# Kernel optimization log

Measured on AMD Instinct MI355X. Metric: run time of the kernel, lower is better.

## Reference

```python
import jax, jax.numpy as jnp
import numpy as np
import math

DIM = 1024
N_HEADS = 16
HEAD_DIM = DIM // N_HEADS
MAX_LEN = 4096
THETA = 10000.0
LN_EPS = 1e-5


def _rope_tables(dim, max_len, theta=THETA):
    # matches precompute_rope: freqs over even indices, angles = outer(t, freqs)
    inv = 1.0 / theta ** (np.arange(0, dim, 2, dtype=np.float32) / dim)
    t = np.arange(max_len, dtype=np.float32)
    ang = np.outer(t, inv)  # [max_len, dim//2]
    return jnp.asarray(np.cos(ang)), jnp.asarray(np.sin(ang))


def setup_inputs() -> dict:
    key = jax.random.key(0)
    ks = jax.random.split(key, 5)
    B, T, D = 2, 2048, DIM
    s = 1.0 / math.sqrt(D)
    x = jax.random.normal(ks[0], (B, T, D), dtype=jnp.float32)
    wq = jax.random.normal(ks[1], (D, D), dtype=jnp.float32) * s
    wk = jax.random.normal(ks[2], (D, D), dtype=jnp.float32) * s
    wv = jax.random.normal(ks[3], (D, D), dtype=jnp.float32) * s
    wo = jax.random.normal(ks[4], (D, D), dtype=jnp.float32) * s
    ln_g = jnp.ones((D,), dtype=jnp.float32)
    ln_b = jnp.zeros((D,), dtype=jnp.float32)
    cos, sin = _rope_tables(HEAD_DIM, MAX_LEN)
    return {"x": x, "wq": wq, "wk": wk, "wv": wv, "wo": wo,
            "ln_g": ln_g, "ln_b": ln_b, "cos": cos, "sin": sin}


def _rotate(x, cos, sin):
    # x: [B, T, H, hd]; complex multiply on interleaved (even, odd) pairs
    B, T, H, hd = x.shape
    xr = x.reshape(B, T, H, hd // 2, 2)
    x0, x1 = xr[..., 0], xr[..., 1]
    c = cos[None, :T, None, :]
    s = sin[None, :T, None, :]
    o0 = x0 * c - x1 * s
    o1 = x0 * s + x1 * c
    return jnp.stack([o0, o1], axis=-1).reshape(B, T, H, hd)


def reference(x, wq, wk, wv, wo, ln_g, ln_b, cos, sin):
    B, T, D = x.shape
    H, hd = N_HEADS, HEAD_DIM
    # LayerNorm
    mu = jnp.mean(x, axis=-1, keepdims=True)
    var = jnp.var(x, axis=-1, keepdims=True)
    h = (x - mu) * jax.lax.rsqrt(var + LN_EPS) * ln_g + ln_b
    # QKV projections (torch Linear: h @ W.T)
    q = jnp.einsum('btd,ed->bte', h, wq).reshape(B, T, H, hd)
    k = jnp.einsum('btd,ed->bte', h, wk).reshape(B, T, H, hd)
    v = jnp.einsum('btd,ed->bte', h, wv).reshape(B, T, H, hd)
    q = _rotate(q, cos, sin)
    k = _rotate(k, cos, sin)
    # full (non-causal) attention, scores [B, H, T, T]
    scores = jnp.einsum('bqhd,bkhd->bhqk', q, k) / math.sqrt(hd)
    attn = jax.nn.softmax(scores, axis=-1)
    out = jnp.einsum('bhqk,bkhd->bqhd', attn, v).reshape(B, T, D)
    return jnp.einsum('btd,ed->bte', out, wo)
```

## Files before the change

kernel.cpp:

```cpp
#include <hip/hip_runtime.h>
#include <hip/hip_bf16.h>

typedef __attribute__((ext_vector_type(4))) float          fx4;
typedef __attribute__((ext_vector_type(8))) __bf16         bfx8;
typedef __attribute__((ext_vector_type(8))) unsigned short usx8;
typedef __attribute__((ext_vector_type(4))) unsigned short usx4;

#define TLEN 2048
#define ROWS 4096
#define D    1024

__device__ __forceinline__ float bf2f(unsigned short u) {
    union { unsigned int i; float f; } v; v.i = ((unsigned int)u) << 16; return v.f;
}
__device__ __forceinline__ unsigned short f2bf(float f) {
    union { float f; unsigned int i; } v; v.f = f;
    unsigned int r = v.i + 0x7fffu + ((v.i >> 16) & 1u);
    return (unsigned short)(r >> 16);
}
__device__ __forceinline__ unsigned int cvtpk_bf16(float lo, float hi) {
    unsigned int r;
    asm("v_cvt_pk_bf16_f32 %0, %1, %2" : "=v"(r) : "v"(lo), "v"(hi));
    return r;
}
__device__ __forceinline__ float fast_cos(float a) {
    float r; asm("v_cos_f32 %0, %1" : "=v"(r) : "v"(a)); return r;
}
__device__ __forceinline__ float fast_sin(float a) {
    float r; asm("v_sin_f32 %0, %1" : "=v"(r) : "v"(a)); return r;
}
__device__ __forceinline__ void gload_lds16(const unsigned short* g, unsigned short* l) {
    __builtin_amdgcn_global_load_lds((const __attribute__((address_space(1))) void*)g,
                                     (__attribute__((address_space(3))) void*)l, 16, 0, 0);
}

__global__ __launch_bounds__(256) void ln_kernel(const float* __restrict__ x,
                                                 const float* __restrict__ g,
                                                 const float* __restrict__ bta,
                                                 unsigned short* __restrict__ hout) {
    const int row = blockIdx.x, tid = threadIdx.x;
    fx4 v = ((const fx4*)(x + (size_t)row * D))[tid];
    float s  = v[0] + v[1] + v[2] + v[3];
    float s2 = v[0]*v[0] + v[1]*v[1] + v[2]*v[2] + v[3]*v[3];
    #pragma unroll
    for (int mk = 32; mk >= 1; mk >>= 1) { s += __shfl_xor(s, mk); s2 += __shfl_xor(s2, mk); }
    __shared__ float red[8];
    const int wave = tid >> 6, lane = tid & 63;
    if (lane == 0) { red[wave] = s; red[4 + wave] = s2; }
    __syncthreads();
    s  = red[0] + red[1] + red[2] + red[3];
    s2 = red[4] + red[5] + red[6] + red[7];
    float mu   = s * (1.0f / D);
    float var  = s2 * (1.0f / D) - mu * mu;
    float rstd = rsqrtf(var + 1e-5f);
    fx4 gv = ((const fx4*)g)[tid];
    fx4 bv = ((const fx4*)bta)[tid];
    usx4 o;
    #pragma unroll
    for (int j = 0; j < 4; j++) o[j] = f2bf((v[j] - mu) * rstd * gv[j] + bv[j]);
    ((usx4*)hout)[(size_t)row * 256 + tid] = o;
}

__device__ __forceinline__ usx4 cvt4(fx4 a) {
    usx4 o;
    #pragma unroll
    for (int j = 0; j < 4; j++) o[j] = f2bf(a[j]);
    return o;
}
__global__ __launch_bounds__(256) void wconv_kernel(const float* __restrict__ wq, const float* __restrict__ wk,
                                                    const float* __restrict__ wv, const float* __restrict__ wo,
                                                    unsigned short* __restrict__ wqkv,
                                                    unsigned short* __restrict__ wob) {
    const int i = blockIdx.x * 256 + threadIdx.x;
    ((usx4*)wqkv)[i]          = cvt4(((const fx4*)wq)[i]);
    ((usx4*)wqkv)[262144 + i] = cvt4(((const fx4*)wk)[i]);
    ((usx4*)wqkv)[524288 + i] = cvt4(((const fx4*)wv)[i]);
    ((usx4*)wob)[i]           = cvt4(((const fx4*)wo)[i]);
}

__global__ __launch_bounds__(256) void qkvt_gemm(const unsigned short* __restrict__ hbuf,
                                                 const unsigned short* __restrict__ wqkv,
                                                 unsigned short* __restrict__ qkout,
                                                 unsigned short* __restrict__ vtout) {
    constexpr int K = 1024;
    __shared__ __align__(16) unsigned short As[128 * 32];
    __shared__ __align__(16) unsigned short Bs[128 * 32];
    const int tid = threadIdx.x, lane = tid & 63, wave = tid >> 6;
    const int fr = lane & 15, fq = lane >> 4;
    const int wr = wave >> 1, wc = wave & 1;

    const int id = blockIdx.x;
    const bool isqk = id < 512;
    int bm, bn;
    const unsigned short *Ab, *Bb;
    if (isqk) {
        bm = id & 31; bn = id >> 5;
        Ab = hbuf + (size_t)(bm * 128) * K;
        Bb = wqkv + (size_t)(bn * 128) * K;
    } else {
        int j = id - 512; bm = j & 7; bn = j >> 3;
        Ab = wqkv + (size_t)(2048 * 1024) + (size_t)(bm * 128) * K;
        Bb = hbuf + (size_t)(bn * 128) * K;
    }

    const int str0 = wave * 32 + (lane >> 2);
    const int stc  = (lane & 3) * 8;

    fx4 acc[4][4];
    #pragma unroll
    for (int m = 0; m < 4; m++)
        #pragma unroll
        for (int n = 0; n < 4; n++) acc[m][n] = (fx4)0.0f;

    for (int kt = 0; kt < K; kt += 32) {
        gload_lds16(Ab + (size_t)str0 * K + kt + stc,        &As[str0 * 32 + stc]);
        gload_lds16(Ab + (size_t)(str0 + 16) * K + kt + stc, &As[(str0 + 16) * 32 + stc]);
        gload_lds16(Bb + (size_t)str0 * K + kt + stc,        &Bs[str0 * 32 + stc]);
        gload_lds16(Bb + (size_t)(str0 + 16) * K + kt + stc, &Bs[(str0 + 16) * 32 + stc]);
        __syncthreads();
        bfx8 aF[4], bF[4];
        #pragma unroll
        for (int m = 0; m < 4; m++) aF[m] = *(const bfx8*)&As[(wr * 64 + m * 16 + fr) * 32 + fq * 8];
        #pragma unroll
        for (int n = 0; n < 4; n++) bF[n] = *(const bfx8*)&Bs[(wc * 64 + n * 16 + fr) * 32 + fq * 8];
        #pragma unroll
        for (int m = 0; m < 4; m++)
            #pragma unroll
            for (int n = 0; n < 4; n++)
                acc[m][n] = __builtin_amdgcn_mfma_f32_16x16x32_bf16(aF[m], bF[n], acc[m][n], 0, 0, 0);
        __syncthreads();
    }

    const int row0 = bm * 128 + wr * 64 + fq * 4;
    const int col0 = bn * 128 + wc * 64 + fr;
    if (isqk) {
        const float QS = 0.125f * 1.44269504088896f;
        const bool isq = bn < 8;
        const float sgn = (fr & 1) ? 1.0f : -1.0f;
        float fp[4];
        #pragma unroll
        for (int n = 0; n < 4; n++) {
            float pif = (float)(n * 8 + (fr >> 1));
            fp[n] = __builtin_amdgcn_exp2f(fmaf(pif, -0.415241011861f, -2.651496129472f));
        }
        #pragma unroll
        for (int m = 0; m < 4; m++) {
            const int rbase = row0 + m * 16;
            const float tf = (float)(rbase & (TLEN - 1));
            #pragma unroll
            for (int n = 0; n < 4; n++) {
                #pragma unroll
                for (int j = 0; j < 4; j++) {
                    float a = __builtin_amdgcn_fractf((tf + (float)j) * fp[n]);
                    float c = fast_cos(a), s = fast_sin(a);
                    float self = acc[m][n][j];
                    float other = __shfl_xor(self, 1);
                    float o = self * c + other * (sgn * s);
                    if (isq) o *= QS;
                    qkout[(size_t)(rbase + j) * 2048 + col0 + n * 16] = f2bf(o);
                }
            }
        }
    } else {
        const int bb = bn >> 4;
        #pragma unroll
        for (int m = 0; m < 4; m++)
            #pragma unroll
            for (int n = 0; n < 4; n++) {
                const int t = (col0 + n * 16) & (TLEN - 1);
                const int tp = (t & ~63) | ((n >> 1) * 32 + ((fr >> 2)) * 8 + ((n & 1)) * 4 + (fr & 3));
                #pragma unroll
                for (int j = 0; j < 4; j++) {
                    const int d = row0 + m * 16 + j;
                    vtout[(((size_t)(bb * 16 + (d >> 6)) * 64) + (d & 63)) * TLEN + tp] = f2bf(acc[m][n][j]);
                }
            }
    }
}

__global__ __launch_bounds__(256) void gemm_out64(const unsigned short* __restrict__ A,
                                                  const unsigned short* __restrict__ B,
                                                  float* __restrict__ C) {
    constexpr int K = 1024;
    __shared__ __align__(16) unsigned short As[128 * 32];
    __shared__ __align__(16) unsigned short Bs[64 * 32];
    const int tid = threadIdx.x, lane = tid & 63, wave = tid >> 6;
    const int fr = lane & 15, fq = lane >> 4;
    const int bm = blockIdx.x, bn = blockIdx.y;
    const int wr = wave >> 1, wc = wave & 1;

    const int strA = wave * 32 + (lane >> 2);
    const int strB = wave * 16 + (lane >> 2);
    const int stc  = (lane & 3) * 8;
    const unsigned short* Ab = A + (size_t)(bm * 128) * K;
    const unsigned short* Bb = B + (size_t)(bn * 64) * K;

    fx4 acc[4][2];
    #pragma unroll
    for (int m = 0; m < 4; m++)
        #pragma unroll
        for (int n = 0; n < 2; n++) acc[m][n] = (fx4)0.0f;

    for (int kt = 0; kt < K; kt += 32) {
        gload_lds16(Ab + (size_t)strA * K + kt + stc,        &As[strA * 32 + stc]);
        gload_lds16(Ab + (size_t)(strA + 16) * K + kt + stc, &As[(strA + 16) * 32 + stc]);
        gload_lds16(Bb + (size_t)strB * K + kt + stc,        &Bs[strB * 32 + stc]);
        __syncthreads();
        bfx8 aF[4], bF[2];
        #pragma unroll
        for (int m = 0; m < 4; m++) aF[m] = *(const bfx8*)&As[(wr * 64 + m * 16 + fr) * 32 + fq * 8];
        #pragma unroll
        for (int n = 0; n < 2; n++) bF[n] = *(const bfx8*)&Bs[(wc * 32 + n * 16 + fr) * 32 + fq * 8];
        #pragma unroll
        for (int m = 0; m < 4; m++)
            #pragma unroll
            for (int n = 0; n < 2; n++)
                acc[m][n] = __builtin_amdgcn_mfma_f32_16x16x32_bf16(aF[m], bF[n], acc[m][n], 0, 0, 0);
        __syncthreads();
    }

    const int row0 = bm * 128 + wr * 64 + fq * 4;
    const int col0 = bn * 64 + wc * 32 + fr;
    #pragma unroll
    for (int m = 0; m < 4; m++)
        #pragma unroll
        for (int n = 0; n < 2; n++)
            #pragma unroll
            for (int j = 0; j < 4; j++)
                C[(size_t)(row0 + m * 16 + j) * 1024 + col0 + n * 16] = acc[m][n][j];
}

__global__ __launch_bounds__(256) void attn_kernel(const unsigned short* __restrict__ qk,
                                                   const unsigned short* __restrict__ vt,
                                                   unsigned short* __restrict__ ao) {
    const int flat = blockIdx.x + (blockIdx.y << 5);
    const int sid  = (flat & 7) * 128 + (flat >> 3);
    const int qt = sid & 31, bh = sid >> 5;
    const int b = bh >> 4, hh = bh & 15;
    const int tid = threadIdx.x, lane = tid & 63, wave = tid >> 6;
    const int fr = lane & 15, fq = lane >> 4;

    __shared__ __align__(16) unsigned short sK[2][64 * 64];
    __shared__ __align__(16) unsigned short sVt[2][64 * 64];

    const size_t rs = 2048;
    const unsigned short* qb  = qk + (size_t)b * TLEN * rs + hh * 64;
    const unsigned short* kb  = qb + 1024;
    const unsigned short* vtb = vt + (size_t)bh * (64 * TLEN);

    bfx8 qF[2];
    {
        int qrow = qt * 64 + wave * 16 + fr;
        const unsigned short* qp = qb + (size_t)qrow * rs + fq * 8;
        qF[0] = *(const bfx8*)qp;
        qF[1] = *(const bfx8*)(qp + 32);
    }
    union { unsigned short us[8]; bfx8 bf; } ones_u;
    #pragma unroll
    for (int i = 0; i < 8; i++) ones_u.us[i] = 0x3F80;

    const int srow = lane >> 3;
    const int scol = ((lane & 7) ^ srow) * 8;

    #pragma unroll
    for (int i = 0; i < 2; i++) {
        int rg = wave * 2 + i;
        gload_lds16(kb  + (size_t)(rg * 8 + srow) * rs + scol,   &sK[0][rg * 512 + lane * 8]);
        gload_lds16(vtb + (size_t)(rg * 8 + srow) * TLEN + scol, &sVt[0][rg * 512 + lane * 8]);
    }

    float m_run = 0.0f;
    fx4 oacc[4];
    fx4 oextra = (fx4)0.0f;
    #pragma unroll
    for (int db = 0; db < 4; db++) oacc[db] = (fx4)0.0f;

    #pragma unroll 2
    for (int t = 0; t < 32; ++t) {
        const int buf = t & 1;
        __syncthreads();

        if (t + 1 < 32) {
            const int kt = (t + 1) * 64;
            #pragma unroll
            for (int i = 0; i < 2; i++) {
                int rg = wave * 2 + i;
                gload_lds16(kb  + (size_t)(kt + rg * 8 + srow) * rs + scol,
                            &sK[buf ^ 1][rg * 512 + lane * 8]);
                gload_lds16(vtb + (size_t)(rg * 8 + srow) * TLEN + kt + scol,
                            &sVt[buf ^ 1][rg * 512 + lane * 8]);
            }
        }

        fx4 sacc[4];
        #pragma unroll
        for (int n = 0; n < 4; n++) sacc[n] = (fx4)(-m_run);
        __builtin_amdgcn_s_setprio(1);
        #pragma unroll
        for (int s = 0; s < 2; s++)
            #pragma unroll
            for (int n = 0; n < 4; n++) {
                bfx8 kF = *(const bfx8*)&sK[buf][(n * 16 + fr) * 64 + (((s * 4 + fq) ^ (fr & 7)) * 8)];
                sacc[n] = __builtin_amdgcn_mfma_f32_16x16x32_bf16(kF, qF[s], sacc[n], 0, 0, 0);
            }
        __builtin_amdgcn_s_setprio(0);

        float t0 = fmaxf(fmaxf(sacc[0][0], sacc[0][1]), sacc[0][2]);
        float t1 = fmaxf(fmaxf(sacc[0][3], sacc[1][0]), sacc[1][1]);
        float t2 = fmaxf(fmaxf(sacc[1][2], sacc[1][3]), sacc[2][0]);
        float t3 = fmaxf(fmaxf(sacc[2][1], sacc[2][2]), sacc[2][3]);
        float t4 = fmaxf(fmaxf(sacc[3][0], sacc[3][1]), sacc[3][2]);
        float smax = fmaxf(fmaxf(fmaxf(t0, t1), t2), fmaxf(fmaxf(t3, t4), sacc[3][3]));
        if (!__all(smax <= 8.0f)) {
            smax = fmaxf(smax, __shfl_xor(smax, 16));
            smax = fmaxf(smax, __shfl_xor(smax, 32));
            float delta = fmaxf(smax, 0.0f);
            float scal = __builtin_amdgcn_exp2f(-delta);
            m_run += delta;
            #pragma unroll
            for (int n = 0; n < 4; n++)
                #pragma unroll
                for (int j = 0; j < 4; j++) sacc[n][j] -= delta;
            #pragma unroll
            for (int db = 0; db < 4; db++) oacc[db] *= scal;
            oextra *= scal;
        }
        float p[4][4];
        #pragma unroll
        for (int n = 0; n < 4; n++)
            #pragma unroll
            for (int j = 0; j < 4; j++)
                p[n][j] = __builtin_amdgcn_exp2f(sacc[n][j]);

        unsigned int u[4][2];
        #pragma unroll
        for (int n = 0; n < 4; n++)
            #pragma unroll
            for (int h = 0; h < 2; h++)
                u[n][h] = cvtpk_bf16(p[n][2 * h], p[n][2 * h + 1]);

        __builtin_amdgcn_s_setprio(1);
        #pragma unroll
        for (int s = 0; s < 2; s++) {
            union { unsigned int ui[4]; bfx8 bf; } cv;
            cv.ui[0] = u[2 * s][0];     cv.ui[1] = u[2 * s][1];
            cv.ui[2] = u[2 * s + 1][0]; cv.ui[3] = u[2 * s + 1][1];
            #pragma unroll
            for (int db = 0; db < 4; db++) {
                bfx8 vF = *(const bfx8*)&sVt[buf][(db * 16 + fr) * 64 + (((s * 4 + fq) ^ (fr & 7)) * 8)];
                oacc[db] = __builtin_amdgcn_mfma_f32_16x16x32_bf16(vF, cv.bf, oacc[db], 0, 0, 0);
            }
            oextra = __builtin_amdgcn_mfma_f32_16x16x32_bf16(ones_u.bf, cv.bf, oextra, 0, 0, 0);
        }
        __builtin_amdgcn_s_setprio(0);
    }

    float invl = 1.0f / oextra[0];
    const int qrow = qt * 64 + wave * 16 + fr;
    unsigned short* aop = ao + (size_t)(b * TLEN + qrow) * 1024 + hh * 64 + fq * 4;
    #pragma unroll
    for (int db = 0; db < 4; db++) {
        usx4 o4;
        #pragma unroll
        for (int j = 0; j < 4; j++) o4[j] = f2bf(oacc[db][j] * invl);
        *(usx4*)(aop + db * 16) = o4;
    }
}

extern "C" void kernel_launch(void* const* d_in, const int* in_sizes, int n_in,
                              void* d_out, int out_size, void* d_ws, size_t ws_size,
                              hipStream_t stream) {
    const float* x    = (const float*)d_in[0];
    const float* wq   = (const float*)d_in[1];
    const float* wk   = (const float*)d_in[2];
    const float* wv   = (const float*)d_in[3];
    const float* wo   = (const float*)d_in[4];
    const float* lng  = (const float*)d_in[5];
    const float* lnb  = (const float*)d_in[6];

    char* ws = (char*)d_ws;
    unsigned short* wob  = (unsigned short*)(ws);
    unsigned short* wqkv = (unsigned short*)(ws + (2u  << 20));
    unsigned short* hbuf = (unsigned short*)(ws + (8u  << 20));
    unsigned short* qk   = (unsigned short*)(ws + (16u << 20));
    unsigned short* vtb  = (unsigned short*)(ws + (32u << 20));
    unsigned short* ao   = (unsigned short*)(ws + (8u  << 20));

    ln_kernel<<<ROWS, 256, 0, stream>>>(x, lng, lnb, hbuf);
    wconv_kernel<<<1024, 256, 0, stream>>>(wq, wk, wv, wo, wqkv, wob);
    qkvt_gemm<<<768, 256, 0, stream>>>(hbuf, wqkv, qk, vtb);
    attn_kernel<<<dim3(32, 32), 256, 0, stream>>>(qk, vtb, ao);
    gemm_out64<<<dim3(32, 16), 256, 0, stream>>>(ao, wob, (float*)d_out);
}
```

Measured before the change: 133.9 us.

## Process two query tiles per attention block and merge LN with weight conversion

Each attention block now handles 128 query rows, two 64-row groups per wave, so every K/V tile staged in LDS and every K/V fragment read is reused for two query groups. This halves the grid to 512 blocks and halves global K/V traffic per query row, at the cost of more registers and possibly lower occupancy. Separately, the LayerNorm and weight bf16 conversion kernels are fused into a single launch to remove one kernel launch gap.

```diff
diff --git a/kernel.cpp b/kernel.cpp
--- a/kernel.cpp
+++ b/kernel.cpp
@@ -34,11 +34,30 @@
                                      (__attribute__((address_space(3))) void*)l, 16, 0, 0);
 }
 
-__global__ __launch_bounds__(256) void ln_kernel(const float* __restrict__ x,
-                                                 const float* __restrict__ g,
-                                                 const float* __restrict__ bta,
-                                                 unsigned short* __restrict__ hout) {
-    const int row = blockIdx.x, tid = threadIdx.x;
+__device__ __forceinline__ usx4 cvt4(fx4 a) {
+    usx4 o;
+    #pragma unroll
+    for (int j = 0; j < 4; j++) o[j] = f2bf(a[j]);
+    return o;
+}
+__global__ __launch_bounds__(256) void prep_kernel(const float* __restrict__ x,
+                                                   const float* __restrict__ g,
+                                                   const float* __restrict__ bta,
+                                                   const float* __restrict__ wq, const float* __restrict__ wk,
+                                                   const float* __restrict__ wv, const float* __restrict__ wo,
+                                                   unsigned short* __restrict__ hout,
+                                                   unsigned short* __restrict__ wqkv,
+                                                   unsigned short* __restrict__ wob) {
+    const int tid = threadIdx.x;
+    if (blockIdx.x >= 4096) {
+        const int i = (blockIdx.x - 4096) * 256 + tid;
+        ((usx4*)wqkv)[i]          = cvt4(((const fx4*)wq)[i]);
+        ((usx4*)wqkv)[262144 + i] = cvt4(((const fx4*)wk)[i]);
+        ((usx4*)wqkv)[524288 + i] = cvt4(((const fx4*)wv)[i]);
+        ((usx4*)wob)[i]           = cvt4(((const fx4*)wo)[i]);
+        return;
+    }
+    const int row = blockIdx.x;
     fx4 v = ((const fx4*)(x + (size_t)row * D))[tid];
     float s  = v[0] + v[1] + v[2] + v[3];
     float s2 = v[0]*v[0] + v[1]*v[1] + v[2]*v[2] + v[3]*v[3];
@@ -61,23 +80,6 @@
     ((usx4*)hout)[(size_t)row * 256 + tid] = o;
 }
 
-__device__ __forceinline__ usx4 cvt4(fx4 a) {
-    usx4 o;
-    #pragma unroll
-    for (int j = 0; j < 4; j++) o[j] = f2bf(a[j]);
-    return o;
-}
-__global__ __launch_bounds__(256) void wconv_kernel(const float* __restrict__ wq, const float* __restrict__ wk,
-                                                    const float* __restrict__ wv, const float* __restrict__ wo,
-                                                    unsigned short* __restrict__ wqkv,
-                                                    unsigned short* __restrict__ wob) {
-    const int i = blockIdx.x * 256 + threadIdx.x;
-    ((usx4*)wqkv)[i]          = cvt4(((const fx4*)wq)[i]);
-    ((usx4*)wqkv)[262144 + i] = cvt4(((const fx4*)wk)[i]);
-    ((usx4*)wqkv)[524288 + i] = cvt4(((const fx4*)wv)[i]);
-    ((usx4*)wob)[i]           = cvt4(((const fx4*)wo)[i]);
-}
-
 __global__ __launch_bounds__(256) void qkvt_gemm(const unsigned short* __restrict__ hbuf,
                                                  const unsigned short* __restrict__ wqkv,
                                                  unsigned short* __restrict__ qkout,
@@ -233,9 +235,9 @@
 __global__ __launch_bounds__(256) void attn_kernel(const unsigned short* __restrict__ qk,
                                                    const unsigned short* __restrict__ vt,
                                                    unsigned short* __restrict__ ao) {
-    const int flat = blockIdx.x + (blockIdx.y << 5);
-    const int sid  = (flat & 7) * 128 + (flat >> 3);
-    const int qt = sid & 31, bh = sid >> 5;
+    const int flat = blockIdx.x + (blockIdx.y << 4);
+    const int sid  = (flat & 7) * 64 + (flat >> 3);
+    const int qt = sid & 15, bh = sid >> 4;
     const int b = bh >> 4, hh = bh & 15;
     const int tid = threadIdx.x, lane = tid & 63, wave = tid >> 6;
     const int fr = lane & 15, fq = lane >> 4;
@@ -248,12 +250,13 @@
     const unsigned short* kb  = qb + 1024;
     const unsigned short* vtb = vt + (size_t)bh * (64 * TLEN);
 
-    bfx8 qF[2];
-    {
-        int qrow = qt * 64 + wave * 16 + fr;
+    bfx8 qF[2][2];
+    #pragma unroll
+    for (int g = 0; g < 2; g++) {
+        int qrow = qt * 128 + g * 64 + wave * 16 + fr;
         const unsigned short* qp = qb + (size_t)qrow * rs + fq * 8;
-        qF[0] = *(const bfx8*)qp;
-        qF[1] = *(const bfx8*)(qp + 32);
+        qF[g][0] = *(const bfx8*)qp;
+        qF[g][1] = *(const bfx8*)(qp + 32);
     }
     union { unsigned short us[8]; bfx8 bf; } ones_u;
     #pragma unroll
@@ -269,11 +272,13 @@
         gload_lds16(vtb + (size_t)(rg * 8 + srow) * TLEN + scol, &sVt[0][rg * 512 + lane * 8]);
     }
 
-    float m_run = 0.0f;
-    fx4 oacc[4];
-    fx4 oextra = (fx4)0.0f;
-    #pragma unroll
-    for (int db = 0; db < 4; db++) oacc[db] = (fx4)0.0f;
+    float m_run[2] = {0.0f, 0.0f};
+    fx4 oacc[2][4];
+    fx4 oextra[2] = {(fx4)0.0f, (fx4)0.0f};
+    #pragma unroll
+    for (int g = 0; g < 2; g++)
+        #pragma unroll
+        for (int db = 0; db < 4; db++) oacc[g][db] = (fx4)0.0f;
 
     #pragma unroll 2
     for (int t = 0; t < 32; ++t) {
@@ -292,78 +297,140 @@
             }
         }
 
-        fx4 sacc[4];
-        #pragma unroll
-        for (int n = 0; n < 4; n++) sacc[n] = (fx4)(-m_run);
+        bfx8 kF[2][4];
+        #pragma unroll
+        for (int s = 0; s < 2; s++)
+            #pragma unroll
+            for (int n = 0; n < 4; n++)
+                kF[s][n] = *(const bfx8*)&sK[buf][(n * 16 + fr) * 64 + (((s * 4 + fq) ^ (fr & 7)) * 8)];
+        fx4 sacc0[4], sacc1[4];
+        #pragma unroll
+        for (int n = 0; n < 4; n++) { sacc0[n] = (fx4)(-m_run[0]); sacc1[n] = (fx4)(-m_run[1]); }
         __builtin_amdgcn_s_setprio(1);
         #pragma unroll
         for (int s = 0; s < 2; s++)
             #pragma unroll
+            for (int n = 0; n < 4; n++)
+                sacc0[n] = __builtin_amdgcn_mfma_f32_16x16x32_bf16(kF[s][n], qF[0][s], sacc0[n], 0, 0, 0);
+        #pragma unroll
+        for (int s = 0; s < 2; s++)
+            #pragma unroll
+            for (int n = 0; n < 4; n++)
+                sacc1[n] = __builtin_amdgcn_mfma_f32_16x16x32_bf16(kF[s][n], qF[1][s], sacc1[n], 0, 0, 0);
+        __builtin_amdgcn_s_setprio(0);
+
+        unsigned int u0[4][2];
+        {
+            float t0 = fmaxf(fmaxf(sacc0[0][0], sacc0[0][1]), sacc0[0][2]);
+            float t1 = fmaxf(fmaxf(sacc0[0][3], sacc0[1][0]), sacc0[1][1]);
+            float t2 = fmaxf(fmaxf(sacc0[1][2], sacc0[1][3]), sacc0[2][0]);
+            float t3 = fmaxf(fmaxf(sacc0[2][1], sacc0[2][2]), sacc0[2][3]);
+            float t4 = fmaxf(fmaxf(sacc0[3][0], sacc0[3][1]), sacc0[3][2]);
+            float smax = fmaxf(fmaxf(fmaxf(t0, t1), t2), fmaxf(fmaxf(t3, t4), sacc0[3][3]));
+            if (!__all(smax <= 8.0f)) {
+                smax = fmaxf(smax, __shfl_xor(smax, 16));
+                smax = fmaxf(smax, __shfl_xor(smax, 32));
+                float delta = fmaxf(smax, 0.0f);
+                float scal = __builtin_amdgcn_exp2f(-delta);
+                m_run[0] += delta;
+                #pragma unroll
+                for (int n = 0; n < 4; n++)
+                    #pragma unroll
+                    for (int j = 0; j < 4; j++) sacc0[n][j] -= delta;
+                #pragma unroll
+                for (int db = 0; db < 4; db++) oacc[0][db] *= scal;
+                oextra[0] *= scal;
+            }
+            #pragma unroll
             for (int n = 0; n < 4; n++) {
-                bfx8 kF = *(const bfx8*)&sK[buf][(n * 16 + fr) * 64 + (((s * 4 + fq) ^ (fr & 7)) * 8)];
-                sacc[n] = __builtin_amdgcn_mfma_f32_16x16x32_bf16(kF, qF[s], sacc[n], 0, 0, 0);
-            }
-        __builtin_amdgcn_s_setprio(0);
-
-        float t0 = fmaxf(fmaxf(sacc[0][0], sacc[0][1]), sacc[0][2]);
-        float t1 = fmaxf(fmaxf(sacc[0][3], sacc[1][0]), sacc[1][1]);
-        float t2 = fmaxf(fmaxf(sacc[1][2], sacc[1][3]), sacc[2][0]);
-        float t3 = fmaxf(fmaxf(sacc[2][1], sacc[2][2]), sacc[2][3]);
-        float t4 = fmaxf(fmaxf(sacc[3][0], sacc[3][1]), sacc[3][2]);
-        float smax = fmaxf(fmaxf(fmaxf(t0, t1), t2), fmaxf(fmaxf(t3, t4), sacc[3][3]));
-        if (!__all(smax <= 8.0f)) {
-            smax = fmaxf(smax, __shfl_xor(smax, 16));
-            smax = fmaxf(smax, __shfl_xor(smax, 32));
-            float delta = fmaxf(smax, 0.0f);
-            float scal = __builtin_amdgcn_exp2f(-delta);
-            m_run += delta;
-            #pragma unroll
-            for (int n = 0; n < 4; n++)
-                #pragma unroll
-                for (int j = 0; j < 4; j++) sacc[n][j] -= delta;
-            #pragma unroll
-            for (int db = 0; db < 4; db++) oacc[db] *= scal;
-            oextra *= scal;
-        }
-        float p[4][4];
-        #pragma unroll
-        for (int n = 0; n < 4; n++)
-            #pragma unroll
-            for (int j = 0; j < 4; j++)
-                p[n][j] = __builtin_amdgcn_exp2f(sacc[n][j]);
-
-        unsigned int u[4][2];
-        #pragma unroll
-        for (int n = 0; n < 4; n++)
-            #pragma unroll
-            for (int h = 0; h < 2; h++)
-                u[n][h] = cvtpk_bf16(p[n][2 * h], p[n][2 * h + 1]);
+                float plo0 = __builtin_amdgcn_exp2f(sacc0[n][0]);
+                float phi0 = __builtin_amdgcn_exp2f(sacc0[n][1]);
+                float plo1 = __builtin_amdgcn_exp2f(sacc0[n][2]);
+                float phi1 = __builtin_amdgcn_exp2f(sacc0[n][3]);
+                u0[n][0] = cvtpk_bf16(plo0, phi0);
+                u0[n][1] = cvtpk_bf16(plo1, phi1);
+            }
+        }
+
+        bfx8 vF[2][4];
+        #pragma unroll
+        for (int s = 0; s < 2; s++)
+            #pragma unroll
+            for (int db = 0; db < 4; db++)
+                vF[s][db] = *(const bfx8*)&sVt[buf][(db * 16 + fr) * 64 + (((s * 4 + fq) ^ (fr & 7)) * 8)];
 
         __builtin_amdgcn_s_setprio(1);
         #pragma unroll
         for (int s = 0; s < 2; s++) {
             union { unsigned int ui[4]; bfx8 bf; } cv;
-            cv.ui[0] = u[2 * s][0];     cv.ui[1] = u[2 * s][1];
-            cv.ui[2] = u[2 * s + 1][0]; cv.ui[3] = u[2 * s + 1][1];
-            #pragma unroll
-            for (int db = 0; db < 4; db++) {
-                bfx8 vF = *(const bfx8*)&sVt[buf][(db * 16 + fr) * 64 + (((s * 4 + fq) ^ (fr & 7)) * 8)];
-                oacc[db] = __builtin_amdgcn_mfma_f32_16x16x32_bf16(vF, cv.bf, oacc[db], 0, 0, 0);
-            }
-            oextra = __builtin_amdgcn_mfma_f32_16x16x32_bf16(ones_u.bf, cv.bf, oextra, 0, 0, 0);
+            cv.ui[0] = u0[2 * s][0];     cv.ui[1] = u0[2 * s][1];
+            cv.ui[2] = u0[2 * s + 1][0]; cv.ui[3] = u0[2 * s + 1][1];
+            #pragma unroll
+            for (int db = 0; db < 4; db++)
+                oacc[0][db] = __builtin_amdgcn_mfma_f32_16x16x32_bf16(vF[s][db], cv.bf, oacc[0][db], 0, 0, 0);
+            oextra[0] = __builtin_amdgcn_mfma_f32_16x16x32_bf16(ones_u.bf, cv.bf, oextra[0], 0, 0, 0);
         }
         __builtin_amdgcn_s_setprio(0);
-    }
-
-    float invl = 1.0f / oextra[0];
-    const int qrow = qt * 64 + wave * 16 + fr;
-    unsigned short* aop = ao + (size_t)(b * TLEN + qrow) * 1024 + hh * 64 + fq * 4;
-    #pragma unroll
-    for (int db = 0; db < 4; db++) {
-        usx4 o4;
-        #pragma unroll
-        for (int j = 0; j < 4; j++) o4[j] = f2bf(oacc[db][j] * invl);
-        *(usx4*)(aop + db * 16) = o4;
+
+        unsigned int u1[4][2];
+        {
+            float t0 = fmaxf(fmaxf(sacc1[0][0], sacc1[0][1]), sacc1[0][2]);
+            float t1 = fmaxf(fmaxf(sacc1[0][3], sacc1[1][0]), sacc1[1][1]);
+            float t2 = fmaxf(fmaxf(sacc1[1][2], sacc1[1][3]), sacc1[2][0]);
+            float t3 = fmaxf(fmaxf(sacc1[2][1], sacc1[2][2]), sacc1[2][3]);
+            float t4 = fmaxf(fmaxf(sacc1[3][0], sacc1[3][1]), sacc1[3][2]);
+            float smax = fmaxf(fmaxf(fmaxf(t0, t1), t2), fmaxf(fmaxf(t3, t4), sacc1[3][3]));
+            if (!__all(smax <= 8.0f)) {
+                smax = fmaxf(smax, __shfl_xor(smax, 16));
+                smax = fmaxf(smax, __shfl_xor(smax, 32));
+                float delta = fmaxf(smax, 0.0f);
+                float scal = __builtin_amdgcn_exp2f(-delta);
+                m_run[1] += delta;
+                #pragma unroll
+                for (int n = 0; n < 4; n++)
+                    #pragma unroll
+                    for (int j = 0; j < 4; j++) sacc1[n][j] -= delta;
+                #pragma unroll
+                for (int db = 0; db < 4; db++) oacc[1][db] *= scal;
+                oextra[1] *= scal;
+            }
+            #pragma unroll
+            for (int n = 0; n < 4; n++) {
+                float plo0 = __builtin_amdgcn_exp2f(sacc1[n][0]);
+                float phi0 = __builtin_amdgcn_exp2f(sacc1[n][1]);
+                float plo1 = __builtin_amdgcn_exp2f(sacc1[n][2]);
+                float phi1 = __builtin_amdgcn_exp2f(sacc1[n][3]);
+                u1[n][0] = cvtpk_bf16(plo0, phi0);
+                u1[n][1] = cvtpk_bf16(plo1, phi1);
+            }
+        }
+
+        __builtin_amdgcn_s_setprio(1);
+        #pragma unroll
+        for (int s = 0; s < 2; s++) {
+            union { unsigned int ui[4]; bfx8 bf; } cv;
+            cv.ui[0] = u1[2 * s][0];     cv.ui[1] = u1[2 * s][1];
+            cv.ui[2] = u1[2 * s + 1][0]; cv.ui[3] = u1[2 * s + 1][1];
+            #pragma unroll
+            for (int db = 0; db < 4; db++)
+                oacc[1][db] = __builtin_amdgcn_mfma_f32_16x16x32_bf16(vF[s][db], cv.bf, oacc[1][db], 0, 0, 0);
+            oextra[1] = __builtin_amdgcn_mfma_f32_16x16x32_bf16(ones_u.bf, cv.bf, oextra[1], 0, 0, 0);
+        }
+        __builtin_amdgcn_s_setprio(0);
+    }
+
+    #pragma unroll
+    for (int g = 0; g < 2; g++) {
+        float invl = 1.0f / oextra[g][0];
+        const int qrow = qt * 128 + g * 64 + wave * 16 + fr;
+        unsigned short* aop = ao + (size_t)(b * TLEN + qrow) * 1024 + hh * 64 + fq * 4;
+        #pragma unroll
+        for (int db = 0; db < 4; db++) {
+            usx4 o4;
+            #pragma unroll
+            for (int j = 0; j < 4; j++) o4[j] = f2bf(oacc[g][db][j] * invl);
+            *(usx4*)(aop + db * 16) = o4;
+        }
     }
 }
 
@@ -386,9 +453,8 @@
     unsigned short* vtb  = (unsigned short*)(ws + (32u << 20));
     unsigned short* ao   = (unsigned short*)(ws + (8u  << 20));
 
-    ln_kernel<<<ROWS, 256, 0, stream>>>(x, lng, lnb, hbuf);
-    wconv_kernel<<<1024, 256, 0, stream>>>(wq, wk, wv, wo, wqkv, wob);
+    prep_kernel<<<5120, 256, 0, stream>>>(x, lng, lnb, wq, wk, wv, wo, hbuf, wqkv, wob);
     qkvt_gemm<<<768, 256, 0, stream>>>(hbuf, wqkv, qk, vtb);
-    attn_kernel<<<dim3(32, 32), 256, 0, stream>>>(qk, vtb, ao);
+    attn_kernel<<<dim3(16, 32), 256, 0, stream>>>(qk, vtb, ao);
     gemm_out64<<<dim3(32, 16), 256, 0, stream>>>(ao, wob, (float*)d_out);
 }
```

After: 127.4 us. 4.8% less time.
